# Kernel tuning notes

Measured on AMD Instinct MI355X. Metric: run time of the kernel, lower is better.

The kernel has to match this reference:

```python
import jax, jax.numpy as jnp
import numpy as np

DIM = 256
FFN_DIM = 512
NH = 8
EPS = 1e-5


def ln(x, g, b):
    m = x.mean(-1, keepdims=True)
    v = ((x - m) ** 2).mean(-1, keepdims=True)
    return (x - m) / jnp.sqrt(v + EPS) * g + b


def setup_inputs() -> dict:
    key = jax.random.key(0)
    ks = jax.random.split(key, 16)
    B, L, C, H, W = 16, 16384, DIM, 128, 128
    s = 0.02
    return {
        "query": jax.random.normal(ks[0], (B, 1, C), jnp.float32),
        "mem": jax.random.normal(ks[1], (B, L, C), jnp.float32),
        "ior_emb": jax.random.uniform(ks[2], (B, NH, H, W), jnp.float32),
        # input_proj: Linear(dim,dim) + ReLU + LayerNorm
        "W_ip": jax.random.normal(ks[3], (C, C), jnp.float32) * s,
        "b_ip": jnp.zeros((C,), jnp.float32),
        "g_ip": jnp.ones((C,), jnp.float32),
        "be_ip": jnp.zeros((C,), jnp.float32),
        # q / kv projections
        "W_q": jax.random.normal(ks[4], (C, C), jnp.float32) * s,
        "b_q": jnp.zeros((C,), jnp.float32),
        "W_kv": jax.random.normal(ks[5], (C, 2 * C), jnp.float32) * s,
        "b_kv": jnp.zeros((2 * C,), jnp.float32),
        # norm_q, norm_ffn
        "g_q": jnp.ones((C,), jnp.float32),
        "be_q": jnp.zeros((C,), jnp.float32),
        "g_f": jnp.ones((C,), jnp.float32),
        "be_f": jnp.zeros((C,), jnp.float32),
        # ffn (Mlp)
        "W1": jax.random.normal(ks[6], (C, FFN_DIM), jnp.float32) * s,
        "b1": jnp.zeros((FFN_DIM,), jnp.float32),
        "W2": jax.random.normal(ks[7], (FFN_DIM, C), jnp.float32) * s,
        "b2": jnp.zeros((C,), jnp.float32),
    }


def reference(query, mem, ior_emb, W_ip, b_ip, g_ip, be_ip, W_q, b_q, W_kv, b_kv,
              g_q, be_q, g_f, be_f, W1, b1, W2, b2):
    B, L, C = mem.shape
    nh = ior_emb.shape[1]
    hd = C // nh
    scale = hd ** -0.5
    # input_proj(mem): Linear -> ReLU -> LayerNorm
    m = ln(jax.nn.relu(mem @ W_ip + b_ip), g_ip, be_ip)  # [B,L,C]
    kv = m @ W_kv + b_kv
    k, v = kv[..., :C], kv[..., C:]
    q = ln(query, g_q, be_q) @ W_q + b_q  # [B,1,C]
    # per-head split along channel == reshape (..., nh, hd)
    qh = q.reshape(B, 1, nh, hd)
    kh = k.reshape(B, L, nh, hd)
    vh = v.reshape(B, L, nh, hd)
    ior = ior_emb.reshape(B, nh, 1, L)
    scores = jnp.einsum('bqhd,blhd->bhql', qh, kh) * scale * ior  # [B,nh,1,L]
    attn = jax.nn.softmax(scores, axis=-1)
    out = jnp.einsum('bhql,blhd->bqhd', attn, vh).reshape(B, 1, C)
    x = out + query
    h = ln(x, g_f, be_f)
    ffn = jax.nn.gelu(h @ W1 + b1, approximate=False) @ W2 + b2
    return x + ffn
```

## Files before the change

kernel.cpp:

```cpp
#include <hip/hip_runtime.h>
#include <math.h>

#define CDIM 256
#define LDIM 16384
#define NH 8
#define HD 32
#define FFN 512
#define EPS 1e-5f
#define SCALE 0.17677669529663687f

#define RB 64
#define NCHUNK 256
#define LDA 264
#define PSTRIDE 258

typedef __attribute__((ext_vector_type(8))) short short8;
typedef __attribute__((ext_vector_type(4))) float f32x4;

union U8 { short8 s8; unsigned u[4]; };

__device__ inline unsigned short f2bf(float x) {
    unsigned int u = __float_as_uint(x);
    unsigned int lsb = (u >> 16) & 1u;
    u += 0x7fffu + lsb;
    return (unsigned short)(u >> 16);
}


__global__ __launch_bounds__(256) void convert_weights(const float* __restrict__ Wip,
                                                       unsigned short* __restrict__ w1) {
    int idx = blockIdx.x * 256 + threadIdx.x;
    int j = idx & 7, l = (idx >> 3) & 63, c = (idx >> 9) & 15, t = idx >> 13;
    int k = t * 32 + (l >> 4) * 8 + j;
    int colc = c * 16 + (l & 15);
    w1[idx] = f2bf(Wip[k * CDIM + colc]);
}


__global__ __launch_bounds__(256) void qprep_kernel(const float* __restrict__ query,
                                                    const float* __restrict__ Wq,
                                                    const float* __restrict__ bq,
                                                    const float* __restrict__ gq,
                                                    const float* __restrict__ beq,
                                                    const float* __restrict__ Wkv,
                                                    const float* __restrict__ bkv,
                                                    float* __restrict__ qs,
                                                    unsigned short* __restrict__ wts,
                                                    float* __restrict__ qcb) {
    int b = blockIdx.x;
    int tid = threadIdx.x;
    int wave = tid >> 6, lane = tid & 63;
    __shared__ float sh[CDIM];
    __shared__ float qsh[CDIM];
    __shared__ float red[8];

    float x = query[b * CDIM + tid];
    float s = x, sq = x * x;
#pragma unroll
    for (int m = 32; m >= 1; m >>= 1) { s += __shfl_xor(s, m, 64); sq += __shfl_xor(sq, m, 64); }
    if (lane == 0) { red[wave] = s; red[4 + wave] = sq; }
    __syncthreads();
    float ts = red[0] + red[1] + red[2] + red[3];
    float tq = red[4] + red[5] + red[6] + red[7];
    float mean = ts * (1.f / CDIM);
    float var = tq * (1.f / CDIM) - mean * mean;
    float rstd = rsqrtf(var + EPS);
    sh[tid] = (x - mean) * rstd * gq[tid] + beq[tid];
    __syncthreads();

    float acc = bq[tid];
    for (int k = 0; k < CDIM; ++k) acc = fmaf(sh[k], Wq[k * CDIM + tid], acc);
    float qv = acc * SCALE;
    qs[b * CDIM + tid] = qv;
    qsh[tid] = qv;
    __syncthreads();

    float wa[8];
#pragma unroll
    for (int h = 0; h < 8; ++h) wa[h] = 0.f;
    const float* wr = Wkv + (size_t)tid * (2 * CDIM);
#pragma unroll
    for (int h = 0; h < 8; ++h)
#pragma unroll
        for (int d = 0; d < 32; ++d)
            wa[h] = fmaf(wr[h * 32 + d], qsh[h * 32 + d], wa[h]);
    unsigned short* wb = wts + (b << 12) + ((tid >> 5) << 9) + (((tid >> 3) & 3) << 7) + (tid & 7);
#pragma unroll
    for (int h = 0; h < 8; ++h) wb[h << 3] = f2bf(wa[h]);
#pragma unroll
    for (int h = 8; h < 16; ++h) wb[h << 3] = 0;

    if (tid < 16) {
        float cb = 0.f;
        if (tid < 8) {
#pragma unroll
            for (int d = 0; d < 32; ++d) cb = fmaf(bkv[tid * 32 + d], qsh[tid * 32 + d], cb);
        }
        qcb[b * 16 + tid] = cb;
    }
}


__device__ inline void mfma_gemm(const unsigned short* __restrict__ smA,
                                 const unsigned short* __restrict__ wsw, int NC, int ctile0,
                                 int lx, int quad, f32x4 acc[4][4]) {
#pragma unroll
    for (int rt = 0; rt < 4; ++rt)
#pragma unroll
        for (int ci = 0; ci < 4; ++ci) acc[rt][ci] = (f32x4){0.f, 0.f, 0.f, 0.f};

    int l = quad * 16 + lx;
#pragma unroll
    for (int t = 0; t < 8; ++t) {
        short8 bfrag[4];
#pragma unroll
        for (int ci = 0; ci < 4; ++ci)
            bfrag[ci] = *(const short8*)(wsw + (((size_t)(t * NC + ctile0 + ci)) * 64 + l) * 8);
        short8 afrag[4];
#pragma unroll
        for (int rt = 0; rt < 4; ++rt)
            afrag[rt] = *(const short8*)(smA + (rt * 16 + lx) * LDA + t * 32 + quad * 8);
#pragma unroll
        for (int rt = 0; rt < 4; ++rt)
#pragma unroll
            for (int ci = 0; ci < 4; ++ci)
                acc[rt][ci] = __builtin_amdgcn_mfma_f32_16x16x32_bf16(afrag[rt], bfrag[ci], acc[rt][ci], 0, 0, 0);
    }
}


__device__ inline void mfma_svec(const unsigned short* __restrict__ smA,
                                 const unsigned short* __restrict__ wt,
                                 int lx, int quad, f32x4 accS[4]) {
#pragma unroll
    for (int rt = 0; rt < 4; ++rt) accS[rt] = (f32x4){0.f, 0.f, 0.f, 0.f};
    int l = quad * 16 + lx;
#pragma unroll
    for (int t = 0; t < 8; ++t) {
        short8 bf = *(const short8*)(wt + ((t * 64 + l) << 3));
        short8 af[4];
#pragma unroll
        for (int rt = 0; rt < 4; ++rt)
            af[rt] = *(const short8*)(smA + (rt * 16 + lx) * LDA + t * 32 + quad * 8);
#pragma unroll
        for (int rt = 0; rt < 4; ++rt)
            accS[rt] = __builtin_amdgcn_mfma_f32_16x16x32_bf16(af[rt], bf, accS[rt], 0, 0, 0);
    }
}


__global__ __launch_bounds__(256, 4) void main_kernel(const float* __restrict__ mem,
                                                      const unsigned short* __restrict__ w1,
                                                      const unsigned short* __restrict__ wts,
                                                      const float* __restrict__ bip,
                                                      const float* __restrict__ gip,
                                                      const float* __restrict__ beip,
                                                      const float* __restrict__ qcb,
                                                      const float* __restrict__ ior,
                                                      float* __restrict__ partials) {
    int blk = blockIdx.x;
    int b = blk >> 8;
    int chunk = blk & 255;
    int row0 = chunk * RB;
    int tid = threadIdx.x;
    int w = tid >> 6, lane = tid & 63;
    int quad = lane >> 4, lx = lane & 15;

    __shared__ unsigned short bufA[RB * LDA];
    __shared__ float iorS[NH][66];
    __shared__ float redS[4][RB];
    __shared__ float redQ[4][RB];
    __shared__ float stats[2][RB];

    {
        int i0 = tid, i1 = tid + 256;
        iorS[i0 >> 6][i0 & 63] = ior[((size_t)(b * NH + (i0 >> 6))) * LDIM + row0 + (i0 & 63)];
        iorS[i1 >> 6][i1 & 63] = ior[((size_t)(b * NH + (i1 >> 6))) * LDIM + row0 + (i1 & 63)];
    }
    {
        const float4* src = (const float4*)(mem + ((size_t)b * LDIM + row0) * CDIM);
#pragma unroll
        for (int it = 0; it < 16; ++it) {
            int i = tid + 256 * it;
            int r = i >> 6, c4 = i & 63;
            float4 v = src[i];
            ushort4 u;
            u.x = f2bf(v.x); u.y = f2bf(v.y); u.z = f2bf(v.z); u.w = f2bf(v.w);
            *(ushort4*)&bufA[r * LDA + c4 * 4] = u;
        }
    }
    __syncthreads();

    int col[4];
#pragma unroll
    for (int ci = 0; ci < 4; ++ci) col[ci] = (4 * w + ci) * 16 + lx;

    f32x4 acc[4][4];
    mfma_gemm(bufA, w1, 16, 4 * w, lx, quad, acc);

    float bb[4], gg[4], ee[4];
#pragma unroll
    for (int ci = 0; ci < 4; ++ci) { bb[ci] = bip[col[ci]]; gg[ci] = gip[col[ci]]; ee[ci] = beip[col[ci]]; }

#pragma unroll
    for (int rt = 0; rt < 4; ++rt) {
#pragma unroll
        for (int reg = 0; reg < 4; ++reg) {
#pragma unroll
            for (int ci = 0; ci < 4; ++ci)
                acc[rt][ci][reg] = fmaxf(acc[rt][ci][reg] + bb[ci], 0.f);
            float s2 = acc[rt][0][reg] + acc[rt][1][reg] + acc[rt][2][reg] + acc[rt][3][reg];
            float q2 = acc[rt][0][reg] * acc[rt][0][reg] + acc[rt][1][reg] * acc[rt][1][reg]
                     + acc[rt][2][reg] * acc[rt][2][reg] + acc[rt][3][reg] * acc[rt][3][reg];
#pragma unroll
            for (int m = 8; m >= 1; m >>= 1) { s2 += __shfl_xor(s2, m, 64); q2 += __shfl_xor(q2, m, 64); }
            if (lx == 0) {
                int row = rt * 16 + quad * 4 + reg;
                redS[w][row] = s2;
                redQ[w][row] = q2;
            }
        }
    }
    __syncthreads();
    if (tid < RB) {
        float s2 = redS[0][tid] + redS[1][tid] + redS[2][tid] + redS[3][tid];
        float q2 = redQ[0][tid] + redQ[1][tid] + redQ[2][tid] + redQ[3][tid];
        float mean = s2 * (1.f / CDIM);
        float var = q2 * (1.f / CDIM) - mean * mean;
        stats[0][tid] = mean;
        stats[1][tid] = rsqrtf(var + EPS);
    }
    __syncthreads();

    unsigned ypk0[4][4], ypk1[4][4];
#pragma unroll
    for (int rt = 0; rt < 4; ++rt) {
        float mn[4], rs[4];
#pragma unroll
        for (int reg = 0; reg < 4; ++reg) {
            int row = rt * 16 + quad * 4 + reg;
            mn[reg] = stats[0][row];
            rs[reg] = stats[1][row];
        }
#pragma unroll
        for (int ci = 0; ci < 4; ++ci) {
            unsigned short u0 = f2bf((acc[rt][ci][0] - mn[0]) * rs[0] * gg[ci] + ee[ci]);
            unsigned short u1 = f2bf((acc[rt][ci][1] - mn[1]) * rs[1] * gg[ci] + ee[ci]);
            unsigned short u2 = f2bf((acc[rt][ci][2] - mn[2]) * rs[2] * gg[ci] + ee[ci]);
            unsigned short u3 = f2bf((acc[rt][ci][3] - mn[3]) * rs[3] * gg[ci] + ee[ci]);
            int rbase = rt * 16 + quad * 4;
            bufA[(rbase + 0) * LDA + col[ci]] = u0;
            bufA[(rbase + 1) * LDA + col[ci]] = u1;
            bufA[(rbase + 2) * LDA + col[ci]] = u2;
            bufA[(rbase + 3) * LDA + col[ci]] = u3;
            ypk0[rt][ci] = (unsigned)u0 | ((unsigned)u1 << 16);
            ypk1[rt][ci] = (unsigned)u2 | ((unsigned)u3 << 16);
        }
    }
    __syncthreads();

    f32x4 accS[4];
    mfma_svec(bufA, wts + ((size_t)b << 12), lx, quad, accS);

    float qcv = qcb[(b << 4) + lx];
    float p[16];
    float cmax = -1e30f;
#pragma unroll
    for (int rt = 0; rt < 4; ++rt)
#pragma unroll
        for (int reg = 0; reg < 4; ++reg) {
            int row = rt * 16 + quad * 4 + reg;
            float sc = (accS[rt][reg] + qcv) * iorS[lx & 7][row];
            p[rt * 4 + reg] = sc;
            cmax = fmaxf(cmax, sc);
        }
    cmax = fmaxf(cmax, __shfl_xor(cmax, 16, 64));
    cmax = fmaxf(cmax, __shfl_xor(cmax, 32, 64));
    float csum = 0.f;
#pragma unroll
    for (int i = 0; i < 16; ++i) { p[i] = __expf(p[i] - cmax); csum += p[i]; }
    csum += __shfl_xor(csum, 16, 64);
    csum += __shfl_xor(csum, 32, 64);

    f32x4 accPV[4];
#pragma unroll
    for (int ci = 0; ci < 4; ++ci) accPV[ci] = (f32x4){0.f, 0.f, 0.f, 0.f};

    int srcA = ((quad & 1) << 5) + lx;
    int srcB = srcA + 16;
    bool hiQ = quad >= 2;
#pragma unroll
    for (int t2 = 0; t2 < 2; ++t2) {
        float pe[8];
#pragma unroll
        for (int jj = 0; jj < 4; ++jj) {
            float v0 = __shfl(p[t2 * 8 + jj], srcA, 64);
            float v1 = __shfl(p[t2 * 8 + 4 + jj], srcA, 64);
            pe[jj] = hiQ ? v1 : v0;
            float v2 = __shfl(p[t2 * 8 + jj], srcB, 64);
            float v3 = __shfl(p[t2 * 8 + 4 + jj], srcB, 64);
            pe[4 + jj] = hiQ ? v3 : v2;
        }
        U8 pa;
        pa.u[0] = (unsigned)f2bf(pe[0]) | ((unsigned)f2bf(pe[1]) << 16);
        pa.u[1] = (unsigned)f2bf(pe[2]) | ((unsigned)f2bf(pe[3]) << 16);
        pa.u[2] = (unsigned)f2bf(pe[4]) | ((unsigned)f2bf(pe[5]) << 16);
        pa.u[3] = (unsigned)f2bf(pe[6]) | ((unsigned)f2bf(pe[7]) << 16);

#pragma unroll
        for (int ci = 0; ci < 4; ++ci) {
            unsigned a0 = (unsigned)__shfl((int)ypk0[t2 * 2][ci], srcA, 64);
            unsigned b0 = (unsigned)__shfl((int)ypk0[t2 * 2 + 1][ci], srcA, 64);
            unsigned a1 = (unsigned)__shfl((int)ypk1[t2 * 2][ci], srcA, 64);
            unsigned b1 = (unsigned)__shfl((int)ypk1[t2 * 2 + 1][ci], srcA, 64);
            unsigned a2 = (unsigned)__shfl((int)ypk0[t2 * 2][ci], srcB, 64);
            unsigned b2 = (unsigned)__shfl((int)ypk0[t2 * 2 + 1][ci], srcB, 64);
            unsigned a3 = (unsigned)__shfl((int)ypk1[t2 * 2][ci], srcB, 64);
            unsigned b3 = (unsigned)__shfl((int)ypk1[t2 * 2 + 1][ci], srcB, 64);
            U8 ub;
            ub.u[0] = hiQ ? b0 : a0;
            ub.u[1] = hiQ ? b1 : a1;
            ub.u[2] = hiQ ? b2 : a2;
            ub.u[3] = hiQ ? b3 : a3;
            accPV[ci] = __builtin_amdgcn_mfma_f32_16x16x32_bf16(pa.s8, ub.s8, accPV[ci], 0, 0, 0);
        }
    }

    size_t pb = ((size_t)(b * NCHUNK + chunk)) * NH * PSTRIDE;
    if (quad < 2) {
#pragma unroll
        for (int reg = 0; reg < 4; ++reg) {
            float* dst = partials + pb + (size_t)(quad * 4 + reg) * PSTRIDE;
#pragma unroll
            for (int ci = 0; ci < 4; ++ci) dst[col[ci]] = accPV[ci][reg];
        }
    }
    if (quad == 0 && lx < 8) {
        float* dst = partials + pb + (size_t)lx * PSTRIDE;
        dst[256] = cmax;
        dst[257] = csum;
    }
}


__global__ __launch_bounds__(256) void combine_kernel(const float* __restrict__ partials,
                                                      const float* __restrict__ Wkv,
                                                      const float* __restrict__ bkv,
                                                      float* __restrict__ attnout) {
    int bh = blockIdx.x;
    int b = bh >> 3, h = bh & 7;
    int tid = threadIdx.x;
    __shared__ float ms[NCHUNK], wf[NCHUNK], mt[CDIM];
    __shared__ float sredA[4];
    __shared__ float ored[8][33];

    const float* base = partials + ((size_t)b * NCHUNK * NH + h) * PSTRIDE;
    ms[tid] = base[(size_t)tid * NH * PSTRIDE + 256];
    __syncthreads();
    float M = -1e30f;
    for (int s = 0; s < NCHUNK; ++s) M = fmaxf(M, ms[s]);
    float e = __expf(ms[tid] - M);
    wf[tid] = e;
    float Sl = base[(size_t)tid * NH * PSTRIDE + 257] * e;
#pragma unroll
    for (int m = 32; m >= 1; m >>= 1) Sl += __shfl_xor(Sl, m, 64);
    if ((tid & 63) == 0) sredA[tid >> 6] = Sl;
    __syncthreads();
    float St = sredA[0] + sredA[1] + sredA[2] + sredA[3];

    float acc = 0.f;
    for (int s = 0; s < NCHUNK; ++s) acc = fmaf(wf[s], base[(size_t)s * NH * PSTRIDE + tid], acc);
    mt[tid] = acc / St;
    __syncthreads();

    int d = tid & 31, g = tid >> 5;
    float a2 = 0.f;
    for (int c = g * 32; c < g * 32 + 32; ++c)
        a2 = fmaf(mt[c], Wkv[(size_t)c * (2 * CDIM) + CDIM + h * 32 + d], a2);
    ored[g][d] = a2;
    __syncthreads();
    if (tid < 32) {
        float o = bkv[CDIM + h * 32 + tid];
#pragma unroll
        for (int gg2 = 0; gg2 < 8; ++gg2) o += ored[gg2][tid];
        attnout[b * CDIM + h * HD + tid] = o;
    }
}


__global__ __launch_bounds__(256) void epilogue_kernel(const float* __restrict__ attnout,
                                                       const float* __restrict__ query,
                                                       const float* __restrict__ gf,
                                                       const float* __restrict__ bef,
                                                       const float* __restrict__ W1,
                                                       const float* __restrict__ b1,
                                                       const float* __restrict__ W2,
                                                       const float* __restrict__ b2,
                                                       float* __restrict__ out) {
    int b = blockIdx.x;
    int tid = threadIdx.x;
    int wave = tid >> 6, lane = tid & 63;
    __shared__ float sh[FFN];
    __shared__ float red[8];

    float x = attnout[b * CDIM + tid] + query[b * CDIM + tid];
    float s = x, sq = x * x;
#pragma unroll
    for (int m = 32; m >= 1; m >>= 1) { s += __shfl_xor(s, m, 64); sq += __shfl_xor(sq, m, 64); }
    if (lane == 0) { red[wave] = s; red[4 + wave] = sq; }
    __syncthreads();
    float ts = red[0] + red[1] + red[2] + red[3];
    float tq = red[4] + red[5] + red[6] + red[7];
    float mean = ts * (1.f / CDIM);
    float var = tq * (1.f / CDIM) - mean * mean;
    float rstd = rsqrtf(var + EPS);
    sh[tid] = (x - mean) * rstd * gf[tid] + bef[tid];
    __syncthreads();

    float t[2];
#pragma unroll
    for (int i = 0; i < 2; ++i) {
        int f = tid + 256 * i;
        float a = b1[f];
        for (int k = 0; k < CDIM; ++k) a = fmaf(sh[k], W1[k * FFN + f], a);
        t[i] = 0.5f * a * (1.f + erff(a * 0.7071067811865476f));
    }
    __syncthreads();
    sh[tid] = t[0];
    sh[tid + 256] = t[1];
    __syncthreads();

    float y = b2[tid];
    for (int f = 0; f < FFN; ++f) y = fmaf(sh[f], W2[f * CDIM + tid], y);
    out[b * CDIM + tid] = x + y;
}


extern "C" void kernel_launch(void* const* d_in, const int* in_sizes, int n_in,
                              void* d_out, int out_size, void* d_ws, size_t ws_size,
                              hipStream_t stream) {
    const float* query = (const float*)d_in[0];
    const float* mem   = (const float*)d_in[1];
    const float* ior   = (const float*)d_in[2];
    const float* Wip   = (const float*)d_in[3];
    const float* bip   = (const float*)d_in[4];
    const float* gip   = (const float*)d_in[5];
    const float* beip  = (const float*)d_in[6];
    const float* Wq    = (const float*)d_in[7];
    const float* bq    = (const float*)d_in[8];
    const float* Wkv   = (const float*)d_in[9];
    const float* bkv   = (const float*)d_in[10];
    const float* gq    = (const float*)d_in[11];
    const float* beq   = (const float*)d_in[12];
    const float* gf    = (const float*)d_in[13];
    const float* bef   = (const float*)d_in[14];
    const float* W1    = (const float*)d_in[15];
    const float* b1    = (const float*)d_in[16];
    const float* W2    = (const float*)d_in[17];
    const float* b2    = (const float*)d_in[18];
    float* out = (float*)d_out;

    char* ws = (char*)d_ws;
    float* qs             = (float*)(ws);
    float* attnout        = (float*)(ws + 16384);
    float* qcb            = (float*)(ws + 32768);
    unsigned short* w1sw  = (unsigned short*)(ws + 33792);
    unsigned short* wtsw  = (unsigned short*)(ws + 164864);
    float* partials       = (float*)(ws + 295936);

    const int B = 16;

    convert_weights<<<256, 256, 0, stream>>>(Wip, w1sw);
    qprep_kernel<<<B, 256, 0, stream>>>(query, Wq, bq, gq, beq, Wkv, bkv, qs, wtsw, qcb);
    main_kernel<<<B * NCHUNK, 256, 0, stream>>>(mem, w1sw, wtsw, bip, gip, beip, qcb, ior, partials);
    combine_kernel<<<B * NH, 256, 0, stream>>>(partials, Wkv, bkv, attnout);
    epilogue_kernel<<<B, 256, 0, stream>>>(attnout, query, gf, bef, W1, b1, W2, b2, out);
}
```

Baseline: 526.5 us.

## Give each wave its own 16-row tile and drop block-wide LayerNorm syncs

Restructures the main kernel so each of the four waves owns 16 rows and computes all 256 output columns. LayerNorm statistics are then reduced inside the wave with shuffles instead of block-wide shared-memory reductions and syncs. The shared tile uses an XOR swizzle instead of padding, and the four waves' partial softmax/PV results are merged in-block before writing a contiguous per-(batch, head, chunk) layout. The combine kernel then reads coalesced data. Each wave now loads the full W_ip fragment set from global memory (16 B-fragments per k-step), which raises weight traffic and register pressure (16 accumulators plus 32 packed values).

```diff
diff --git a/kernel.cpp b/kernel.cpp
--- a/kernel.cpp
+++ b/kernel.cpp
@@ -9,10 +9,7 @@
 #define EPS 1e-5f
 #define SCALE 0.17677669529663687f
 
-#define RB 64
 #define NCHUNK 256
-#define LDA 264
-#define PSTRIDE 258
 
 typedef __attribute__((ext_vector_type(8))) short short8;
 typedef __attribute__((ext_vector_type(4))) float f32x4;
@@ -101,54 +98,6 @@
 }
 
 
-__device__ inline void mfma_gemm(const unsigned short* __restrict__ smA,
-                                 const unsigned short* __restrict__ wsw, int NC, int ctile0,
-                                 int lx, int quad, f32x4 acc[4][4]) {
-#pragma unroll
-    for (int rt = 0; rt < 4; ++rt)
-#pragma unroll
-        for (int ci = 0; ci < 4; ++ci) acc[rt][ci] = (f32x4){0.f, 0.f, 0.f, 0.f};
-
-    int l = quad * 16 + lx;
-#pragma unroll
-    for (int t = 0; t < 8; ++t) {
-        short8 bfrag[4];
-#pragma unroll
-        for (int ci = 0; ci < 4; ++ci)
-            bfrag[ci] = *(const short8*)(wsw + (((size_t)(t * NC + ctile0 + ci)) * 64 + l) * 8);
-        short8 afrag[4];
-#pragma unroll
-        for (int rt = 0; rt < 4; ++rt)
-            afrag[rt] = *(const short8*)(smA + (rt * 16 + lx) * LDA + t * 32 + quad * 8);
-#pragma unroll
-        for (int rt = 0; rt < 4; ++rt)
-#pragma unroll
-            for (int ci = 0; ci < 4; ++ci)
-                acc[rt][ci] = __builtin_amdgcn_mfma_f32_16x16x32_bf16(afrag[rt], bfrag[ci], acc[rt][ci], 0, 0, 0);
-    }
-}
-
-
-__device__ inline void mfma_svec(const unsigned short* __restrict__ smA,
-                                 const unsigned short* __restrict__ wt,
-                                 int lx, int quad, f32x4 accS[4]) {
-#pragma unroll
-    for (int rt = 0; rt < 4; ++rt) accS[rt] = (f32x4){0.f, 0.f, 0.f, 0.f};
-    int l = quad * 16 + lx;
-#pragma unroll
-    for (int t = 0; t < 8; ++t) {
-        short8 bf = *(const short8*)(wt + ((t * 64 + l) << 3));
-        short8 af[4];
-#pragma unroll
-        for (int rt = 0; rt < 4; ++rt)
-            af[rt] = *(const short8*)(smA + (rt * 16 + lx) * LDA + t * 32 + quad * 8);
-#pragma unroll
-        for (int rt = 0; rt < 4; ++rt)
-            accS[rt] = __builtin_amdgcn_mfma_f32_16x16x32_bf16(af[rt], bf, accS[rt], 0, 0, 0);
-    }
-}
-
-
 __global__ __launch_bounds__(256, 4) void main_kernel(const float* __restrict__ mem,
                                                       const unsigned short* __restrict__ w1,
                                                       const unsigned short* __restrict__ wts,
@@ -157,193 +106,204 @@
                                                       const float* __restrict__ beip,
                                                       const float* __restrict__ qcb,
                                                       const float* __restrict__ ior,
-                                                      float* __restrict__ partials) {
+                                                      float* __restrict__ mpart,
+                                                      float* __restrict__ msum) {
     int blk = blockIdx.x;
     int b = blk >> 8;
     int chunk = blk & 255;
-    int row0 = chunk * RB;
     int tid = threadIdx.x;
     int w = tid >> 6, lane = tid & 63;
     int quad = lane >> 4, lx = lane & 15;
 
-    __shared__ unsigned short bufA[RB * LDA];
-    __shared__ float iorS[NH][66];
-    __shared__ float redS[4][RB];
-    __shared__ float redQ[4][RB];
-    __shared__ float stats[2][RB];
+    __shared__ unsigned short bufA[4][4096];
+    __shared__ float iorS[4][NH][17];
+    __shared__ float msL[4][2][8];
+
+    int row0 = chunk * 64 + w * 16;
+    unsigned short* myT = &bufA[w][0];
+    char* myC = (char*)myT;
+    const unsigned short* wtb = wts + ((size_t)b << 12);
+    float qcv = qcb[(b << 4) + lx];
+    int xv = (lx & 7) << 4;
 
     {
-        int i0 = tid, i1 = tid + 256;
-        iorS[i0 >> 6][i0 & 63] = ior[((size_t)(b * NH + (i0 >> 6))) * LDIM + row0 + (i0 & 63)];
-        iorS[i1 >> 6][i1 & 63] = ior[((size_t)(b * NH + (i1 >> 6))) * LDIM + row0 + (i1 & 63)];
+        int hh = lane >> 3, rr = lane & 7;
+        iorS[w][hh][rr]     = ior[((size_t)(b * NH + hh)) * LDIM + row0 + rr];
+        iorS[w][hh][8 + rr] = ior[((size_t)(b * NH + hh)) * LDIM + row0 + 8 + rr];
     }
     {
         const float4* src = (const float4*)(mem + ((size_t)b * LDIM + row0) * CDIM);
-#pragma unroll
-        for (int it = 0; it < 16; ++it) {
-            int i = tid + 256 * it;
-            int r = i >> 6, c4 = i & 63;
-            float4 v = src[i];
+        float4 v[8];
+#pragma unroll
+        for (int it = 0; it < 8; ++it) v[it] = src[it * 64 + lane];
+#pragma unroll
+        for (int it = 0; it < 8; ++it) {
             ushort4 u;
-            u.x = f2bf(v.x); u.y = f2bf(v.y); u.z = f2bf(v.z); u.w = f2bf(v.w);
-            *(ushort4*)&bufA[r * LDA + c4 * 4] = u;
-        }
-    }
-    __syncthreads();
-
-    int col[4];
-#pragma unroll
-    for (int ci = 0; ci < 4; ++ci) col[ci] = (4 * w + ci) * 16 + lx;
-
-    f32x4 acc[4][4];
-    mfma_gemm(bufA, w1, 16, 4 * w, lx, quad, acc);
-
-    float bb[4], gg[4], ee[4];
-#pragma unroll
-    for (int ci = 0; ci < 4; ++ci) { bb[ci] = bip[col[ci]]; gg[ci] = gip[col[ci]]; ee[ci] = beip[col[ci]]; }
-
-#pragma unroll
-    for (int rt = 0; rt < 4; ++rt) {
+            u.x = f2bf(v[it].x); u.y = f2bf(v[it].y); u.z = f2bf(v[it].z); u.w = f2bf(v[it].w);
+            *(ushort4*)(myC + it * 512 + ((lane << 3) ^ ((it & 7) << 4))) = u;
+        }
+#pragma unroll
+        for (int it = 0; it < 8; ++it) v[it] = src[(8 + it) * 64 + lane];
+#pragma unroll
+        for (int it = 0; it < 8; ++it) {
+            ushort4 u;
+            u.x = f2bf(v[it].x); u.y = f2bf(v[it].y); u.z = f2bf(v[it].z); u.w = f2bf(v[it].w);
+            *(ushort4*)(myC + (8 + it) * 512 + ((lane << 3) ^ ((it & 7) << 4))) = u;
+        }
+    }
+    __asm volatile("" ::: "memory");
+
+    f32x4 acc[16];
+#pragma unroll
+    for (int ci = 0; ci < 16; ++ci) acc[ci] = (f32x4){0.f, 0.f, 0.f, 0.f};
+    __builtin_amdgcn_s_setprio(1);
+#pragma unroll
+    for (int t = 0; t < 8; ++t) {
+        short8 af = *(const short8*)(myC + lx * 512 + ((t * 64 + quad * 16) ^ xv));
+#pragma unroll
+        for (int ci = 0; ci < 16; ++ci) {
+            short8 bf = *(const short8*)(w1 + (((size_t)(t * 16 + ci)) * 64 + lane) * 8);
+            acc[ci] = __builtin_amdgcn_mfma_f32_16x16x32_bf16(af, bf, acc[ci], 0, 0, 0);
+        }
+    }
+    __builtin_amdgcn_s_setprio(0);
+
+    f32x4 s2 = (f32x4){0.f, 0.f, 0.f, 0.f};
+    f32x4 q2 = (f32x4){0.f, 0.f, 0.f, 0.f};
+#pragma unroll
+    for (int ci = 0; ci < 16; ++ci) {
+        float bb = bip[ci * 16 + lx];
 #pragma unroll
         for (int reg = 0; reg < 4; ++reg) {
-#pragma unroll
-            for (int ci = 0; ci < 4; ++ci)
-                acc[rt][ci][reg] = fmaxf(acc[rt][ci][reg] + bb[ci], 0.f);
-            float s2 = acc[rt][0][reg] + acc[rt][1][reg] + acc[rt][2][reg] + acc[rt][3][reg];
-            float q2 = acc[rt][0][reg] * acc[rt][0][reg] + acc[rt][1][reg] * acc[rt][1][reg]
-                     + acc[rt][2][reg] * acc[rt][2][reg] + acc[rt][3][reg] * acc[rt][3][reg];
-#pragma unroll
-            for (int m = 8; m >= 1; m >>= 1) { s2 += __shfl_xor(s2, m, 64); q2 += __shfl_xor(q2, m, 64); }
-            if (lx == 0) {
-                int row = rt * 16 + quad * 4 + reg;
-                redS[w][row] = s2;
-                redQ[w][row] = q2;
-            }
-        }
-    }
-    __syncthreads();
-    if (tid < RB) {
-        float s2 = redS[0][tid] + redS[1][tid] + redS[2][tid] + redS[3][tid];
-        float q2 = redQ[0][tid] + redQ[1][tid] + redQ[2][tid] + redQ[3][tid];
-        float mean = s2 * (1.f / CDIM);
-        float var = q2 * (1.f / CDIM) - mean * mean;
-        stats[0][tid] = mean;
-        stats[1][tid] = rsqrtf(var + EPS);
-    }
-    __syncthreads();
-
-    unsigned ypk0[4][4], ypk1[4][4];
-#pragma unroll
-    for (int rt = 0; rt < 4; ++rt) {
-        float mn[4], rs[4];
-#pragma unroll
-        for (int reg = 0; reg < 4; ++reg) {
-            int row = rt * 16 + quad * 4 + reg;
-            mn[reg] = stats[0][row];
-            rs[reg] = stats[1][row];
-        }
-#pragma unroll
-        for (int ci = 0; ci < 4; ++ci) {
-            unsigned short u0 = f2bf((acc[rt][ci][0] - mn[0]) * rs[0] * gg[ci] + ee[ci]);
-            unsigned short u1 = f2bf((acc[rt][ci][1] - mn[1]) * rs[1] * gg[ci] + ee[ci]);
-            unsigned short u2 = f2bf((acc[rt][ci][2] - mn[2]) * rs[2] * gg[ci] + ee[ci]);
-            unsigned short u3 = f2bf((acc[rt][ci][3] - mn[3]) * rs[3] * gg[ci] + ee[ci]);
-            int rbase = rt * 16 + quad * 4;
-            bufA[(rbase + 0) * LDA + col[ci]] = u0;
-            bufA[(rbase + 1) * LDA + col[ci]] = u1;
-            bufA[(rbase + 2) * LDA + col[ci]] = u2;
-            bufA[(rbase + 3) * LDA + col[ci]] = u3;
-            ypk0[rt][ci] = (unsigned)u0 | ((unsigned)u1 << 16);
-            ypk1[rt][ci] = (unsigned)u2 | ((unsigned)u3 << 16);
-        }
-    }
-    __syncthreads();
-
-    f32x4 accS[4];
-    mfma_svec(bufA, wts + ((size_t)b << 12), lx, quad, accS);
-
-    float qcv = qcb[(b << 4) + lx];
-    float p[16];
+            float v = fmaxf(acc[ci][reg] + bb, 0.f);
+            acc[ci][reg] = v;
+            s2[reg] += v;
+            q2[reg] += v * v;
+        }
+    }
+    float mn[4], rs[4];
+#pragma unroll
+    for (int reg = 0; reg < 4; ++reg) {
+        float s = s2[reg], q = q2[reg];
+#pragma unroll
+        for (int m = 8; m >= 1; m >>= 1) { s += __shfl_xor(s, m, 64); q += __shfl_xor(q, m, 64); }
+        float mean = s * (1.f / CDIM);
+        float var = q * (1.f / CDIM) - mean * mean;
+        mn[reg] = mean;
+        rs[reg] = rsqrtf(var + EPS);
+    }
+
+    unsigned ypk0[16], ypk1[16];
+#pragma unroll
+    for (int ci = 0; ci < 16; ++ci) {
+        float g = gip[ci * 16 + lx], e = beip[ci * 16 + lx];
+        unsigned short u0 = f2bf((acc[ci][0] - mn[0]) * rs[0] * g + e);
+        unsigned short u1 = f2bf((acc[ci][1] - mn[1]) * rs[1] * g + e);
+        unsigned short u2 = f2bf((acc[ci][2] - mn[2]) * rs[2] * g + e);
+        unsigned short u3 = f2bf((acc[ci][3] - mn[3]) * rs[3] * g + e);
+        int cb = (ci * 16 + lx) * 2;
+        int r0 = quad * 4;
+        *(unsigned short*)(myC + (r0 + 0) * 512 + (cb ^ (((r0 + 0) & 7) << 4))) = u0;
+        *(unsigned short*)(myC + (r0 + 1) * 512 + (cb ^ (((r0 + 1) & 7) << 4))) = u1;
+        *(unsigned short*)(myC + (r0 + 2) * 512 + (cb ^ (((r0 + 2) & 7) << 4))) = u2;
+        *(unsigned short*)(myC + (r0 + 3) * 512 + (cb ^ (((r0 + 3) & 7) << 4))) = u3;
+        ypk0[ci] = (unsigned)u0 | ((unsigned)u1 << 16);
+        ypk1[ci] = (unsigned)u2 | ((unsigned)u3 << 16);
+    }
+    __asm volatile("" ::: "memory");
+
+    f32x4 accS = (f32x4){0.f, 0.f, 0.f, 0.f};
+#pragma unroll
+    for (int t = 0; t < 8; ++t) {
+        short8 bf = *(const short8*)(wtb + ((t * 64 + lane) << 3));
+        short8 af = *(const short8*)(myC + lx * 512 + ((t * 64 + quad * 16) ^ xv));
+        accS = __builtin_amdgcn_mfma_f32_16x16x32_bf16(af, bf, accS, 0, 0, 0);
+    }
+
+    float pr[4];
     float cmax = -1e30f;
 #pragma unroll
-    for (int rt = 0; rt < 4; ++rt)
-#pragma unroll
-        for (int reg = 0; reg < 4; ++reg) {
-            int row = rt * 16 + quad * 4 + reg;
-            float sc = (accS[rt][reg] + qcv) * iorS[lx & 7][row];
-            p[rt * 4 + reg] = sc;
-            cmax = fmaxf(cmax, sc);
-        }
+    for (int reg = 0; reg < 4; ++reg) {
+        float sc = (accS[reg] + qcv) * iorS[w][lx & 7][quad * 4 + reg];
+        pr[reg] = sc;
+        cmax = fmaxf(cmax, sc);
+    }
     cmax = fmaxf(cmax, __shfl_xor(cmax, 16, 64));
     cmax = fmaxf(cmax, __shfl_xor(cmax, 32, 64));
     float csum = 0.f;
 #pragma unroll
-    for (int i = 0; i < 16; ++i) { p[i] = __expf(p[i] - cmax); csum += p[i]; }
+    for (int reg = 0; reg < 4; ++reg) { pr[reg] = __expf(pr[reg] - cmax); csum += pr[reg]; }
     csum += __shfl_xor(csum, 16, 64);
     csum += __shfl_xor(csum, 32, 64);
 
-    f32x4 accPV[4];
-#pragma unroll
-    for (int ci = 0; ci < 4; ++ci) accPV[ci] = (f32x4){0.f, 0.f, 0.f, 0.f};
-
-    int srcA = ((quad & 1) << 5) + lx;
-    int srcB = srcA + 16;
-    bool hiQ = quad >= 2;
-#pragma unroll
-    for (int t2 = 0; t2 < 2; ++t2) {
+    U8 pa;
+    {
         float pe[8];
 #pragma unroll
-        for (int jj = 0; jj < 4; ++jj) {
-            float v0 = __shfl(p[t2 * 8 + jj], srcA, 64);
-            float v1 = __shfl(p[t2 * 8 + 4 + jj], srcA, 64);
-            pe[jj] = hiQ ? v1 : v0;
-            float v2 = __shfl(p[t2 * 8 + jj], srcB, 64);
-            float v3 = __shfl(p[t2 * 8 + 4 + jj], srcB, 64);
-            pe[4 + jj] = hiQ ? v3 : v2;
-        }
-        U8 pa;
+        for (int j = 0; j < 8; ++j) {
+            int srcl = ((((quad & 1) << 1) + (j >> 2)) << 4) | lx;
+            float v = __shfl(pr[j & 3], srcl, 64);
+            pe[j] = (quad < 2) ? v : 0.f;
+        }
         pa.u[0] = (unsigned)f2bf(pe[0]) | ((unsigned)f2bf(pe[1]) << 16);
         pa.u[1] = (unsigned)f2bf(pe[2]) | ((unsigned)f2bf(pe[3]) << 16);
         pa.u[2] = (unsigned)f2bf(pe[4]) | ((unsigned)f2bf(pe[5]) << 16);
         pa.u[3] = (unsigned)f2bf(pe[6]) | ((unsigned)f2bf(pe[7]) << 16);
-
-#pragma unroll
-        for (int ci = 0; ci < 4; ++ci) {
-            unsigned a0 = (unsigned)__shfl((int)ypk0[t2 * 2][ci], srcA, 64);
-            unsigned b0 = (unsigned)__shfl((int)ypk0[t2 * 2 + 1][ci], srcA, 64);
-            unsigned a1 = (unsigned)__shfl((int)ypk1[t2 * 2][ci], srcA, 64);
-            unsigned b1 = (unsigned)__shfl((int)ypk1[t2 * 2 + 1][ci], srcA, 64);
-            unsigned a2 = (unsigned)__shfl((int)ypk0[t2 * 2][ci], srcB, 64);
-            unsigned b2 = (unsigned)__shfl((int)ypk0[t2 * 2 + 1][ci], srcB, 64);
-            unsigned a3 = (unsigned)__shfl((int)ypk1[t2 * 2][ci], srcB, 64);
-            unsigned b3 = (unsigned)__shfl((int)ypk1[t2 * 2 + 1][ci], srcB, 64);
-            U8 ub;
-            ub.u[0] = hiQ ? b0 : a0;
-            ub.u[1] = hiQ ? b1 : a1;
-            ub.u[2] = hiQ ? b2 : a2;
-            ub.u[3] = hiQ ? b3 : a3;
-            accPV[ci] = __builtin_amdgcn_mfma_f32_16x16x32_bf16(pa.s8, ub.s8, accPV[ci], 0, 0, 0);
-        }
-    }
-
-    size_t pb = ((size_t)(b * NCHUNK + chunk)) * NH * PSTRIDE;
-    if (quad < 2) {
-#pragma unroll
-        for (int reg = 0; reg < 4; ++reg) {
-            float* dst = partials + pb + (size_t)(quad * 4 + reg) * PSTRIDE;
-#pragma unroll
-            for (int ci = 0; ci < 4; ++ci) dst[col[ci]] = accPV[ci][reg];
+    }
+    float* myF = (float*)myT;
+#pragma unroll
+    for (int ci = 0; ci < 16; ++ci) {
+        U8 ub;
+#pragma unroll
+        for (int jj = 0; jj < 4; ++jj) {
+            int srcl = ((((quad & 1) << 1) + (jj >> 1)) << 4) | lx;
+            unsigned vv = (unsigned)__shfl((int)((jj & 1) ? ypk1[ci] : ypk0[ci]), srcl, 64);
+            ub.u[jj] = vv;
+        }
+        f32x4 apv = (f32x4){0.f, 0.f, 0.f, 0.f};
+        apv = __builtin_amdgcn_mfma_f32_16x16x32_bf16(pa.s8, ub.s8, apv, 0, 0, 0);
+        if (quad < 2) {
+#pragma unroll
+            for (int reg = 0; reg < 4; ++reg) {
+                int h = quad * 4 + reg;
+                myF[h * 256 + ci * 16 + lx] = apv[reg];
+            }
         }
     }
     if (quad == 0 && lx < 8) {
-        float* dst = partials + pb + (size_t)lx * PSTRIDE;
-        dst[256] = cmax;
-        dst[257] = csum;
-    }
-}
-
-
-__global__ __launch_bounds__(256) void combine_kernel(const float* __restrict__ partials,
+        msL[w][0][lx] = cmax;
+        msL[w][1][lx] = csum;
+    }
+    __syncthreads();
+
+    {
+        int h = tid >> 5, cg = tid & 31;
+        float m0 = msL[0][0][h], m1 = msL[1][0][h], m2 = msL[2][0][h], m3 = msL[3][0][h];
+        float mm = fmaxf(fmaxf(m0, m1), fmaxf(m2, m3));
+        float e0 = __expf(m0 - mm), e1 = __expf(m1 - mm), e2 = __expf(m2 - mm), e3 = __expf(m3 - mm);
+        float Sc = e0 * msL[0][1][h] + e1 * msL[1][1][h] + e2 * msL[2][1][h] + e3 * msL[3][1][h];
+        const float* f0 = (const float*)&bufA[0][0];
+        const float* f1 = (const float*)&bufA[1][0];
+        const float* f2 = (const float*)&bufA[2][0];
+        const float* f3 = (const float*)&bufA[3][0];
+        size_t obase = ((((size_t)(b * NH + h)) * NCHUNK + chunk) << 8);
+#pragma unroll
+        for (int c = 0; c < 8; ++c) {
+            int idx = h * 256 + cg * 8 + c;
+            float vv = e0 * f0[idx] + e1 * f1[idx] + e2 * f2[idx] + e3 * f3[idx];
+            mpart[obase + cg * 8 + c] = vv;
+        }
+        if (cg == 0) {
+            float* d = msum + (((((size_t)(b * NH + h)) * NCHUNK + chunk)) << 1);
+            d[0] = mm;
+            d[1] = Sc;
+        }
+    }
+}
+
+
+__global__ __launch_bounds__(256) void combine_kernel(const float* __restrict__ mpart,
+                                                      const float* __restrict__ msum,
                                                       const float* __restrict__ Wkv,
                                                       const float* __restrict__ bkv,
                                                       float* __restrict__ attnout) {
@@ -354,14 +314,15 @@
     __shared__ float sredA[4];
     __shared__ float ored[8][33];
 
-    const float* base = partials + ((size_t)b * NCHUNK * NH + h) * PSTRIDE;
-    ms[tid] = base[(size_t)tid * NH * PSTRIDE + 256];
+    const float* basem = mpart + (((size_t)(b * NH + h)) * NCHUNK << 8);
+    const float* bases = msum + (((size_t)(b * NH + h)) * NCHUNK << 1);
+    ms[tid] = bases[tid << 1];
     __syncthreads();
     float M = -1e30f;
     for (int s = 0; s < NCHUNK; ++s) M = fmaxf(M, ms[s]);
     float e = __expf(ms[tid] - M);
     wf[tid] = e;
-    float Sl = base[(size_t)tid * NH * PSTRIDE + 257] * e;
+    float Sl = bases[(tid << 1) + 1] * e;
 #pragma unroll
     for (int m = 32; m >= 1; m >>= 1) Sl += __shfl_xor(Sl, m, 64);
     if ((tid & 63) == 0) sredA[tid >> 6] = Sl;
@@ -369,7 +330,7 @@
     float St = sredA[0] + sredA[1] + sredA[2] + sredA[3];
 
     float acc = 0.f;
-    for (int s = 0; s < NCHUNK; ++s) acc = fmaf(wf[s], base[(size_t)s * NH * PSTRIDE + tid], acc);
+    for (int s = 0; s < NCHUNK; ++s) acc = fmaf(wf[s], basem[((size_t)s << 8) + tid], acc);
     mt[tid] = acc / St;
     __syncthreads();
 
@@ -466,13 +427,14 @@
     float* qcb            = (float*)(ws + 32768);
     unsigned short* w1sw  = (unsigned short*)(ws + 33792);
     unsigned short* wtsw  = (unsigned short*)(ws + 164864);
-    float* partials       = (float*)(ws + 295936);
+    float* mpart          = (float*)(ws + 295936);
+    float* msum           = (float*)(ws + 295936 + 33554432);
 
     const int B = 16;
 
     convert_weights<<<256, 256, 0, stream>>>(Wip, w1sw);
     qprep_kernel<<<B, 256, 0, stream>>>(query, Wq, bq, gq, beq, Wkv, bkv, qs, wtsw, qcb);
-    main_kernel<<<B * NCHUNK, 256, 0, stream>>>(mem, w1sw, wtsw, bip, gip, beip, qcb, ior, partials);
-    combine_kernel<<<B * NH, 256, 0, stream>>>(partials, Wkv, bkv, attnout);
+    main_kernel<<<B * NCHUNK, 256, 0, stream>>>(mem, w1sw, wtsw, bip, gip, beip, qcb, ior, mpart, msum);
+    combine_kernel<<<B * NH, 256, 0, stream>>>(mpart, msum, Wkv, bkv, attnout);
     epilogue_kernel<<<B, 256, 0, stream>>>(attnout, query, gf, bef, W1, b1, W2, b2, out);
 }
```

Result: slower. 553.7 us (+5.2%).
